# Optimization experiments

Measured on AMD Instinct MI355X. Metric: run time of the kernel, lower is better.

Reference implementation:

```python
import jax, jax.numpy as jnp
import numpy as np

N, E, F_IN, G = 50000, 800000, 128, 256
LAYERS = [(128, 4, 64), (256, 4, 64), (256, 1, 64)]  # (fan_in, heads, per-head dim)


def setup_inputs() -> dict:
    key = jax.random.key(0)
    ks = iter(jax.random.split(key, 64))
    nrm = lambda shp, s=1.0: jax.random.normal(next(ks), shp, jnp.float32) * s
    d = {}
    d["x"] = nrm((N, F_IN))
    d["edge_index"] = jax.random.randint(next(ks), (2, E), 0, N, dtype=jnp.int32)
    d["batch"] = jnp.sort(jax.random.randint(next(ks), (N,), 0, G, dtype=jnp.int32))
    for i, (fin, h, c) in enumerate(LAYERS):
        d[f"w{i}"] = nrm((fin, h * c), 1.0 / np.sqrt(fin))
        d[f"asrc{i}"] = nrm((h, c), 0.1)
        d[f"adst{i}"] = nrm((h, c), 0.1)
        d[f"b{i}"] = nrm((h * c,), 0.1)
        d[f"g{i}"] = 1.0 + nrm((h * c,), 0.1)
        d[f"be{i}"] = nrm((h * c,), 0.1)
        d[f"m{i}"] = nrm((h * c,), 0.1)
        d[f"v{i}"] = jnp.abs(nrm((h * c,), 0.1)) + 1.0
    d["fc1w"] = nrm((192, 64), 1.0 / np.sqrt(192)); d["fc1b"] = nrm((64,), 0.1)
    d["fc2w"] = nrm((64, 32), 1.0 / np.sqrt(64));   d["fc2b"] = nrm((32,), 0.1)
    d["fc3w"] = nrm((32, 1), 1.0 / np.sqrt(32));    d["fc3b"] = nrm((1,), 0.1)
    return d


def _gat_layer(x, w, a_s, a_d, b, src, dst, n, heads):
    c = w.shape[1] // heads
    h = (x @ w).reshape(n, heads, c)                      # [N,H,C]
    al_s = jnp.sum(h * a_s[None], axis=-1)                # [N,H]
    al_d = jnp.sum(h * a_d[None], axis=-1)                # [N,H]
    e = jax.nn.leaky_relu(al_s[src] + al_d[dst], 0.2)     # [E',H]
    emax = jax.ops.segment_max(e, dst, num_segments=n)
    emax = jnp.where(jnp.isfinite(emax), emax, 0.0)
    ee = jnp.exp(e - emax[dst])
    den = jax.ops.segment_sum(ee, dst, num_segments=n)
    alpha = ee / (den[dst] + 1e-16)                       # edge softmax per dst node
    out = jax.ops.segment_sum(h[src] * alpha[..., None], dst, num_segments=n)
    return out.reshape(n, heads * c) + b


def _bn(x, g, be, m, v):
    return (x - m) * jax.lax.rsqrt(v + 1e-5) * g + be


def reference(x, edge_index, batch,
              w0, asrc0, adst0, b0, g0, be0, m0, v0,
              w1, asrc1, adst1, b1, g1, be1, m1, v1,
              w2, asrc2, adst2, b2, g2, be2, m2, v2,
              fc1w, fc1b, fc2w, fc2b, fc3w, fc3b):
    n = x.shape[0]
    loop = jnp.arange(n, dtype=edge_index.dtype)          # add_self_loops (PyG default)
    src = jnp.concatenate([edge_index[0], loop])
    dst = jnp.concatenate([edge_index[1], loop])
    layers = [(w0, asrc0, adst0, b0, g0, be0, m0, v0, 4),
              (w1, asrc1, adst1, b1, g1, be1, m1, v1, 4),
              (w2, asrc2, adst2, b2, g2, be2, m2, v2, 1)]
    for (w, a_s, a_d, b, g, be, m, v, heads) in layers:
        x = _gat_layer(x, w, a_s, a_d, b, src, dst, n, heads)
        x = jax.nn.elu(_bn(x, g, be, m, v))
    # multi-pool readout over graphs
    xsum = jax.ops.segment_sum(x, batch, num_segments=G)
    cnt = jax.ops.segment_sum(jnp.ones((n, 1), x.dtype), batch, num_segments=G)
    xmean = xsum / jnp.maximum(cnt, 1.0)
    xmax = jax.ops.segment_max(x, batch, num_segments=G)
    xmax = jnp.where(jnp.isfinite(xmax), xmax, 0.0)
    h = jnp.concatenate([xmean, xmax, xsum], axis=1)      # [G, 192]
    h = jax.nn.relu(h @ fc1w + fc1b)
    h = jax.nn.relu(h @ fc2w + fc2b)
    return h @ fc3w + fc3b                                # [G, 1]
```

## Files before the change

### kernel.cpp

```cpp
#include <hip/hip_runtime.h>
#include <hip/hip_fp16.h>

typedef unsigned short ushort_t;
typedef unsigned int uint_t;
typedef __attribute__((ext_vector_type(8))) _Float16 half8;
typedef __attribute__((ext_vector_type(4))) float f32x4;

#define NN 50000
#define NE 800000
#define NGR 256

typedef __attribute__((address_space(3))) unsigned int as3_u32;
typedef const __attribute__((address_space(1))) unsigned int as1_u32c;
__device__ __forceinline__ void gld16(const ushort_t* g, void* lds_base) {
    __builtin_amdgcn_global_load_lds((as1_u32c*)g, (as3_u32*)lds_base, 16, 0, 0);
}

__global__ void k_scan1(const int* __restrict__ deg, int* __restrict__ rowp,
                        int* __restrict__ bsum, int M) {
    __shared__ int sm[256];
    int t = threadIdx.x, i = blockIdx.x * 256 + t;
    int v = (i < M) ? deg[i] + 1 : 0;
    sm[t] = v; __syncthreads();
    for (int off = 1; off < 256; off <<= 1) {
        int x = (t >= off) ? sm[t - off] : 0;
        __syncthreads();
        sm[t] += x;
        __syncthreads();
    }
    if (i < M) rowp[i] = sm[t] - v;
    if (t == 255) bsum[blockIdx.x] = sm[255];
}

__global__ void k_scan2(int* bsum, int NB) {
    __shared__ int sm[256];
    int t = threadIdx.x;
    int v = (t < NB) ? bsum[t] : 0;
    sm[t] = v; __syncthreads();
    for (int off = 1; off < 256; off <<= 1) {
        int x = (t >= off) ? sm[t - off] : 0;
        __syncthreads();
        sm[t] += x;
        __syncthreads();
    }
    if (t < NB) bsum[t] = sm[t] - v;
}

__global__ void k_scan3(int* rowp, const int* __restrict__ bsum, int* __restrict__ cur,
                        int* __restrict__ colv, int M, int total) {
    int i = blockIdx.x * 256 + threadIdx.x;
    if (i < M) {
        int rp = rowp[i] + bsum[blockIdx.x];
        rowp[i] = rp;
        colv[rp] = i;
        cur[i] = rp + 1;
    }
    if (i == 0) rowp[M] = total;
}

__global__ void k_prep(const float* __restrict__ x0, __half* __restrict__ xf,
                       const float* __restrict__ W0, const float* __restrict__ W1,
                       const float* __restrict__ W2, __half* __restrict__ th,
                       const int* __restrict__ edst, int* __restrict__ deg) {
    int i = blockIdx.x * 256 + threadIdx.x;
    if (i < 1600000) {
        float4 v = ((const float4*)x0)[i];
        __half2 a = __floats2half2_rn(v.x, v.y);
        __half2 b = __floats2half2_rn(v.z, v.w);
        *(__half2*)(xf + i * 4) = a;
        *(__half2*)(xf + i * 4 + 2) = b;
    } else if (i < 1600000 + 114688) {
        int w = i - 1600000;
        const float* W; int K, NC, idx, base;
        if (w < 32768)      { W = W0; K = 128; NC = 256; idx = w;         base = 0; }
        else if (w < 98304) { W = W1; K = 256; NC = 256; idx = w - 32768; base = 32768; }
        else                { W = W2; K = 256; NC = 64;  idx = w - 98304; base = 98304; }
        int k = idx / NC, n = idx % NC;
        th[base + n * K + k] = __float2half(W[idx]);
    } else if (i < 1600000 + 114688 + NE) {
        atomicAdd(&deg[edst[i - 1714688]], 1);
    }
}

template<int KD, int BN>
__device__ __forceinline__ void gemm_body(int bx, int by,
    const __half* __restrict__ Ax, const __half* __restrict__ Bth,
    __half* __restrict__ Hout, const float* __restrict__ a_s,
    const float* __restrict__ a_d, float* __restrict__ als,
    float* __restrict__ ald, int H, int M, int NC) {
    constexpr int BM = 128, BK = 32;
    __shared__ ushort_t sA[BM * BK];
    __shared__ ushort_t sB[BN * BK];
    const int tid = threadIdx.x;
    const int m0 = bx * BM;
    const int n0 = by * BN;
    const int wv = tid >> 6, ln = tid & 63;
    const int lrow = ln & 15, lq = ln >> 4;
    constexpr int RT = (BN == 128) ? 4 : 2;
    int wm, wn;
    if constexpr (BN == 128) { wm = (wv >> 1) * 64; wn = (wv & 1) * 64; }
    else                     { wm = wv * 32;        wn = 0; }
    const int roff = ln >> 2;
    const int coff = (ln & 3) * 8;

    f32x4 acc[RT][4] = {};

    for (int k0 = 0; k0 < KD; k0 += BK) {
        #pragma unroll
        for (int ch = 0; ch < 2; ++ch) {
            int rb = wv * 32 + ch * 16;
            size_t ga = (size_t)(m0 + rb + roff) * KD + k0 + coff;
            gld16((const ushort_t*)Ax + ga, &sA[rb * BK]);
        }
        if constexpr (BN == 128) {
            #pragma unroll
            for (int ch = 0; ch < 2; ++ch) {
                int rb = wv * 32 + ch * 16;
                size_t gb = (size_t)(n0 + rb + roff) * KD + k0 + coff;
                gld16((const ushort_t*)Bth + gb, &sB[rb * BK]);
            }
        } else {
            int rb = wv * 16;
            size_t gb = (size_t)(n0 + rb + roff) * KD + k0 + coff;
            gld16((const ushort_t*)Bth + gb, &sB[rb * BK]);
        }
        __syncthreads();
        half8 af[RT], bf[4];
        #pragma unroll
        for (int r = 0; r < RT; ++r)
            af[r] = *(const half8*)&sA[(wm + r * 16 + lrow) * BK + lq * 8];
        #pragma unroll
        for (int c = 0; c < 4; ++c)
            bf[c] = *(const half8*)&sB[(wn + c * 16 + lrow) * BK + lq * 8];
        #pragma unroll
        for (int r = 0; r < RT; ++r)
            #pragma unroll
            for (int c = 0; c < 4; ++c)
                acc[r][c] = __builtin_amdgcn_mfma_f32_16x16x32_f16(af[r], bf[c], acc[r][c], 0, 0, 0);
        __syncthreads();
    }
    #pragma unroll
    for (int r = 0; r < RT; ++r) {
        #pragma unroll
        for (int c = 0; c < 4; ++c) {
            int colg = n0 + wn + c * 16 + lrow;
            #pragma unroll
            for (int j = 0; j < 4; ++j) {
                int row = m0 + wm + r * 16 + lq * 4 + j;
                if (row < M) Hout[(size_t)row * NC + colg] = __float2half(acc[r][c][j]);
            }
        }
    }
    int hh = (n0 + wn) >> 6;
    float asv[4], adv[4];
    #pragma unroll
    for (int c = 0; c < 4; ++c) {
        int cg = (n0 + wn + c * 16 + lrow) & 63;
        asv[c] = a_s[hh * 64 + cg];
        adv[c] = a_d[hh * 64 + cg];
    }
    #pragma unroll
    for (int r = 0; r < RT; ++r) {
        #pragma unroll
        for (int j = 0; j < 4; ++j) {
            float ts = 0.f, td = 0.f;
            #pragma unroll
            for (int c = 0; c < 4; ++c) {
                float v = acc[r][c][j];
                ts += v * asv[c];
                td += v * adv[c];
            }
            #pragma unroll
            for (int m = 1; m < 16; m <<= 1) {
                ts += __shfl_xor(ts, m);
                td += __shfl_xor(td, m);
            }
            int row = m0 + wm + r * 16 + lq * 4 + j;
            if (lrow == 0 && row < M) {
                als[row * H + hh] = ts;
                ald[row * H + hh] = td;
            }
        }
    }
}

template<int KD, int BN>
__global__ __launch_bounds__(256)
void k_mgemm(const __half* __restrict__ Ax, const __half* __restrict__ Bth,
             __half* __restrict__ Hout,
             const float* __restrict__ a_s, const float* __restrict__ a_d,
             float* __restrict__ als, float* __restrict__ ald,
             int H, int M, int NC) {
    gemm_body<KD, BN>(blockIdx.x, blockIdx.y, Ax, Bth, Hout, a_s, a_d, als, ald, H, M, NC);
}

__global__ __launch_bounds__(256)
void k_gf(const __half* __restrict__ Ax, const __half* __restrict__ Bth,
          __half* __restrict__ Hout,
          const float* __restrict__ a_s, const float* __restrict__ a_d,
          float* __restrict__ als, float* __restrict__ ald, int M,
          const int* __restrict__ esrc, const int* __restrict__ edst,
          int* __restrict__ cur, int* __restrict__ colv) {
    if (blockIdx.x < 782) {
        gemm_body<128, 128>(blockIdx.x >> 1, blockIdx.x & 1, Ax, Bth, Hout,
                            a_s, a_d, als, ald, 4, M, 256);
    } else {
        int fid = blockIdx.x - 782;
        int r = blockIdx.x & 7;
        int c = fid >> 3;
        int base = c * 1024 + (int)threadIdx.x * 4;
        if (base < NE) {
            int4 dv = *(const int4*)(edst + base);
            int4 sv = *(const int4*)(esrc + base);
            const int lo = r * 6250;
            const int* dp = (const int*)&dv;
            const int* sp = (const int*)&sv;
            #pragma unroll
            for (int j = 0; j < 4; ++j) {
                int d = dp[j];
                if ((unsigned)(d - lo) < 6250u) {
                    int pos = atomicAdd(&cur[d], 1);
                    colv[pos] = sp[j];
                }
            }
        }
    }
}

template<int H>
__global__ __launch_bounds__(256)
void k_att(const float* __restrict__ als, const float* __restrict__ ald,
           const int* __restrict__ rowp, const int* __restrict__ colv,
           __half* __restrict__ alpha, float* __restrict__ invb, int M) {
    int node = blockIdx.x * 16 + (threadIdx.x >> 4);
    if (node >= M) return;
    int l = threadIdx.x & 15;
    int rs = rowp[node], re = rowp[node + 1];
    if constexpr (H == 4) {
        float4 ad = *(const float4*)(ald + node * 4);
        float d0 = 0.f, d1 = 0.f, d2 = 0.f, d3 = 0.f;
        for (int i = rs + l; i < re; i += 16) {
            int s = colv[i];
            float4 av = *(const float4*)(als + s * 4);
            float e0 = av.x + ad.x; e0 = e0 > 0.f ? e0 : 0.2f * e0; e0 = __expf(e0);
            float e1 = av.y + ad.y; e1 = e1 > 0.f ? e1 : 0.2f * e1; e1 = __expf(e1);
            float e2 = av.z + ad.z; e2 = e2 > 0.f ? e2 : 0.2f * e2; e2 = __expf(e2);
            float e3 = av.w + ad.w; e3 = e3 > 0.f ? e3 : 0.2f * e3; e3 = __expf(e3);
            d0 += e0; d1 += e1; d2 += e2; d3 += e3;
            __half2 p0 = __floats2half2_rn(e0, e1);
            __half2 p1 = __floats2half2_rn(e2, e3);
            uint2 pk;
            pk.x = *(uint_t*)&p0; pk.y = *(uint_t*)&p1;
            *(uint2*)(alpha + (size_t)i * 4) = pk;
        }
        #pragma unroll
        for (int off = 1; off < 16; off <<= 1) {
            d0 += __shfl_xor(d0, off); d1 += __shfl_xor(d1, off);
            d2 += __shfl_xor(d2, off); d3 += __shfl_xor(d3, off);
        }
        if (l == 0)
            *(float4*)(invb + node * 4) = make_float4(1.f / (d0 + 1e-16f), 1.f / (d1 + 1e-16f),
                                                      1.f / (d2 + 1e-16f), 1.f / (d3 + 1e-16f));
    } else {
        float ad = ald[node];
        float d = 0.f;
        for (int i = rs + l; i < re; i += 16) {
            int s = colv[i];
            float e = als[s] + ad; e = e > 0.f ? e : 0.2f * e; e = __expf(e);
            d += e;
            alpha[i] = __float2half(e);
        }
        #pragma unroll
        for (int off = 1; off < 16; off <<= 1) d += __shfl_xor(d, off);
        if (l == 0) invb[node] = 1.f / (d + 1e-16f);
    }
}

template<int H, bool SPLIT>
__global__ __launch_bounds__(256)
void k_agg(const __half* __restrict__ h, const __half* __restrict__ alpha,
           const float* __restrict__ invb, const int* __restrict__ rowp,
           const int* __restrict__ colv,
           const float* __restrict__ bias, const float* __restrict__ gam,
           const float* __restrict__ bet, const float* __restrict__ mu,
           const float* __restrict__ var,
           __half* __restrict__ xo, float* __restrict__ xf, int M) {
    constexpr int HC = H * 64;
    constexpr int EG = 512 / HC;
    constexpr int L  = 64 / EG;
    constexpr int UN = (H == 4) ? 4 : 2;
    int node = blockIdx.x * 4 + (threadIdx.x >> 6);
    if (node >= M) return;
    int lane = threadIdx.x & 63;
    int rs = rowp[node], re = rowp[node + 1];
    int l = lane & (L - 1), eg = lane / L;
    int hB = (l * 8) >> 6;
    const ushort_t* ab = (const ushort_t*)alpha;
    float acc[8] = {};
    for (int i = rs; i < re; i += EG * UN) {
        #pragma unroll
        for (int k = 0; k < UN; ++k) {
            int idx = i + eg + k * EG;
            bool vld = idx < re;
            int idx2 = vld ? idx : rs;
            int s = colv[idx2];
            ushort_t abits;
            if constexpr (H == 4) abits = ab[(size_t)idx2 * 4 + hB];
            else                  abits = ab[idx2];
            float a = __half2float(__ushort_as_half(vld ? abits : (ushort_t)0));
            uint4 hv = *(const uint4*)(h + (size_t)s * HC + l * 8);
            const __half* hp = (const __half*)&hv;
            #pragma unroll
            for (int j = 0; j < 8; ++j)
                acc[j] = fmaf(a, __half2float(hp[j]), acc[j]);
        }
    }
    #pragma unroll
    for (int off = L; off < 64; off <<= 1) {
        #pragma unroll
        for (int j = 0; j < 8; ++j) acc[j] += __shfl_xor(acc[j], off);
    }
    if (eg == 0) {
        float inv = (H == 4) ? invb[node * 4 + hB] : invb[node];
        float fo[8];
        #pragma unroll
        for (int j = 0; j < 8; ++j) {
            int d = l * 8 + j;
            float o = acc[j] * inv + bias[d];
            float bn = (o - mu[d]) * rsqrtf(var[d] + 1e-5f) * gam[d] + bet[d];
            fo[j] = bn > 0.f ? bn : (__expf(bn) - 1.f);
        }
        if constexpr (SPLIT) {
            __half2 p0 = __floats2half2_rn(fo[0], fo[1]);
            __half2 p1 = __floats2half2_rn(fo[2], fo[3]);
            __half2 p2 = __floats2half2_rn(fo[4], fo[5]);
            __half2 p3 = __floats2half2_rn(fo[6], fo[7]);
            uint4 pk;
            pk.x = *(uint_t*)&p0; pk.y = *(uint_t*)&p1;
            pk.z = *(uint_t*)&p2; pk.w = *(uint_t*)&p3;
            *(uint4*)&xo[(size_t)node * HC + l * 8] = pk;
        } else {
            *(float4*)&xf[(size_t)node * HC + l * 8] = make_float4(fo[0], fo[1], fo[2], fo[3]);
            *(float4*)&xf[(size_t)node * HC + l * 8 + 4] = make_float4(fo[4], fo[5], fo[6], fo[7]);
        }
    }
}

__global__ __launch_bounds__(512)
void k_poolfc(const float* __restrict__ x, const int* __restrict__ batch,
              const float* __restrict__ fc1w, const float* __restrict__ fc1b,
              const float* __restrict__ fc2w, const float* __restrict__ fc2b,
              const float* __restrict__ fc3w, const float* __restrict__ fc3b,
              float* __restrict__ out, int M) {
    __shared__ float ssum[8][64];
    __shared__ float smax[8][64];
    __shared__ float hb[192];
    __shared__ float h1[64];
    __shared__ float h2[32];
    int g = blockIdx.x, t = threadIdx.x;
    int d = t & 63, sub = t >> 6;
    int lo = 0, hi = M;
    while (lo < hi) { int mid = (lo + hi) >> 1; if (batch[mid] < g) lo = mid + 1; else hi = mid; }
    int s = lo;
    lo = 0; hi = M;
    while (lo < hi) { int mid = (lo + hi) >> 1; if (batch[mid] < g + 1) lo = mid + 1; else hi = mid; }
    int e = lo;
    float sum = 0.f, mx = -3.0e38f;
    for (int n = s + sub; n < e; n += 8) {
        float v = x[(size_t)n * 64 + d];
        sum += v; mx = fmaxf(mx, v);
    }
    ssum[sub][d] = sum; smax[sub][d] = mx;
    __syncthreads();
    if (t < 64) {
        float sm = 0.f, m2 = -3.0e38f;
        #pragma unroll
        for (int k = 0; k < 8; ++k) { sm += ssum[k][t]; m2 = fmaxf(m2, smax[k][t]); }
        int cnt = e - s;
        hb[t] = sm / (float)(cnt > 1 ? cnt : 1);
        hb[64 + t] = (cnt == 0) ? 0.f : m2;
        hb[128 + t] = sm;
    }
    __syncthreads();
    if (t < 64) {
        float s1 = fc1b[t];
        for (int k = 0; k < 192; ++k) s1 += hb[k] * fc1w[k * 64 + t];
        h1[t] = fmaxf(s1, 0.f);
    }
    __syncthreads();
    if (t < 32) {
        float s2 = fc2b[t];
        for (int k = 0; k < 64; ++k) s2 += h1[k] * fc2w[k * 32 + t];
        h2[t] = fmaxf(s2, 0.f);
    }
    __syncthreads();
    if (t == 0) {
        float s3 = fc3b[0];
        for (int k = 0; k < 32; ++k) s3 += h2[k] * fc3w[k];
        out[g] = s3;
    }
}

extern "C" void kernel_launch(void* const* d_in, const int* in_sizes, int n_in,
                              void* d_out, int out_size, void* d_ws, size_t ws_size,
                              hipStream_t stream) {
    const float* x0     = (const float*)d_in[0];
    const int* ei       = (const int*)d_in[1];
    const int* batch    = (const int*)d_in[2];
    const float* W[3]   = {(const float*)d_in[3],  (const float*)d_in[11], (const float*)d_in[19]};
    const float* AS[3]  = {(const float*)d_in[4],  (const float*)d_in[12], (const float*)d_in[20]};
    const float* AD[3]  = {(const float*)d_in[5],  (const float*)d_in[13], (const float*)d_in[21]};
    const float* BI[3]  = {(const float*)d_in[6],  (const float*)d_in[14], (const float*)d_in[22]};
    const float* GA[3]  = {(const float*)d_in[7],  (const float*)d_in[15], (const float*)d_in[23]};
    const float* BE[3]  = {(const float*)d_in[8],  (const float*)d_in[16], (const float*)d_in[24]};
    const float* MU[3]  = {(const float*)d_in[9],  (const float*)d_in[17], (const float*)d_in[25]};
    const float* VA[3]  = {(const float*)d_in[10], (const float*)d_in[18], (const float*)d_in[26]};
    const float* fc1w = (const float*)d_in[27];
    const float* fc1b = (const float*)d_in[28];
    const float* fc2w = (const float*)d_in[29];
    const float* fc2b = (const float*)d_in[30];
    const float* fc3w = (const float*)d_in[31];
    const float* fc3b = (const float*)d_in[32];

    char* ws = (char*)d_ws;
    int*   rowp   = (int*)  (ws);
    int*   colv   = (int*)  (ws + 200704);
    int*   bsum   = (int*)  (ws + 3600704);
    float* als    = (float*)(ws + 3602432);
    float* ald    = (float*)(ws + 4402432);
    __half* wTh   = (__half*)(ws + 5202432);
    __half* h_buf = (__half*)(ws + 5661184);
    __half* xf16  = (__half*)(ws + 31261184);
    float* xpool  = (float*)(ws + 56885760);
    __half* alpha = (__half*)(ws + 69685760);
    float* invb   = (float*)(ws + 83285760);
    int*   cur    = (int*)  (ws + 84085760);

    const int* esrc = ei;
    const int* edst = ei + NE;
    const int NB_SCAN = (NN + 255) / 256;

    hipMemsetAsync(cur, 0, NN * sizeof(int), stream);
    k_prep<<<(1600000 + 114688 + NE + 255) / 256, 256, 0, stream>>>(x0, xf16, W[0], W[1], W[2],
                                                                    wTh, edst, cur);
    k_scan1<<<NB_SCAN, 256, 0, stream>>>(cur, rowp, bsum, NN);
    k_scan2<<<1, 256, 0, stream>>>(bsum, NB_SCAN);
    k_scan3<<<NB_SCAN, 256, 0, stream>>>(rowp, bsum, cur, colv, NN, NE + NN);

    const int GB = (NN + 127) / 128;
    const int FILLB = ((NE + 1023) / 1024) * 8;
    int nwb = (NN + 3) / 4;
    int nab = (NN + 15) / 16;

    k_gf<<<782 + FILLB, 256, 0, stream>>>(xf16, wTh, h_buf, AS[0], AD[0], als, ald, NN,
                                          esrc, edst, cur, colv);
    k_att<4><<<nab, 256, 0, stream>>>(als, ald, rowp, colv, alpha, invb, NN);
    k_agg<4, true><<<nwb, 256, 0, stream>>>(h_buf, alpha, invb, rowp, colv,
                                            BI[0], GA[0], BE[0], MU[0], VA[0],
                                            xf16, nullptr, NN);
    k_mgemm<256, 128><<<dim3(GB, 2), 256, 0, stream>>>(xf16, wTh + 32768, h_buf,
                                                       AS[1], AD[1], als, ald, 4, NN, 256);
    k_att<4><<<nab, 256, 0, stream>>>(als, ald, rowp, colv, alpha, invb, NN);
    k_agg<4, true><<<nwb, 256, 0, stream>>>(h_buf, alpha, invb, rowp, colv,
                                            BI[1], GA[1], BE[1], MU[1], VA[1],
                                            xf16, nullptr, NN);
    k_mgemm<256, 64><<<dim3(GB, 1), 256, 0, stream>>>(xf16, wTh + 98304, h_buf,
                                                      AS[2], AD[2], als, ald, 1, NN, 64);
    k_att<1><<<nab, 256, 0, stream>>>(als, ald, rowp, colv, alpha, invb, NN);
    k_agg<1, false><<<nwb, 256, 0, stream>>>(h_buf, alpha, invb, rowp, colv,
                                             BI[2], GA[2], BE[2], MU[2], VA[2],
                                             nullptr, xpool, NN);

    k_poolfc<<<NGR, 512, 0, stream>>>(xpool, batch, fc1w, fc1b, fc2w, fc2b, fc3w, fc3b,
                                      (float*)d_out, NN);
    (void)in_sizes; (void)n_in; (void)out_size; (void)ws_size;
}
```

Measured before the change: 459.4 us.

## Restructure GAT aggregation to full-wavefront rows with readlane-broadcast edge indices

The aggregation kernel now assigns the whole 64-lane wavefront to one node's feature row instead of splitting lanes into edge groups. Each batch of up to 64 neighbour indices and attention weights is loaded cooperatively, then broadcast lane by lane with readlane, with 8 gathers in flight at a time. This removes the cross-lane shuffle reduction and the redundant per-lane colv/alpha loads, but makes each lane's gather narrower (8 or 2 bytes) and puts edges in series within a wavefront. The SPLIT template path is dropped: H==4 always writes half output and H==1 always writes float output.

```diff
diff --git a/kernel.cpp b/kernel.cpp
--- a/kernel.cpp
+++ b/kernel.cpp
@@ -286,63 +286,112 @@
            const float* __restrict__ var,
            __half* __restrict__ xo, float* __restrict__ xf, int M) {
     constexpr int HC = H * 64;
-    constexpr int EG = 512 / HC;
-    constexpr int L  = 64 / EG;
-    constexpr int UN = (H == 4) ? 4 : 2;
     int node = blockIdx.x * 4 + (threadIdx.x >> 6);
     if (node >= M) return;
-    int lane = threadIdx.x & 63;
+    int l = threadIdx.x & 63;
     int rs = rowp[node], re = rowp[node + 1];
-    int l = lane & (L - 1), eg = lane / L;
-    int hB = (l * 8) >> 6;
-    const ushort_t* ab = (const ushort_t*)alpha;
-    float acc[8] = {};
-    for (int i = rs; i < re; i += EG * UN) {
-        #pragma unroll
-        for (int k = 0; k < UN; ++k) {
-            int idx = i + eg + k * EG;
-            bool vld = idx < re;
-            int idx2 = vld ? idx : rs;
-            int s = colv[idx2];
-            ushort_t abits;
-            if constexpr (H == 4) abits = ab[(size_t)idx2 * 4 + hB];
-            else                  abits = ab[idx2];
-            float a = __half2float(__ushort_as_half(vld ? abits : (ushort_t)0));
-            uint4 hv = *(const uint4*)(h + (size_t)s * HC + l * 8);
-            const __half* hp = (const __half*)&hv;
-            #pragma unroll
-            for (int j = 0; j < 8; ++j)
-                acc[j] = fmaf(a, __half2float(hp[j]), acc[j]);
-        }
-    }
-    #pragma unroll
-    for (int off = L; off < 64; off <<= 1) {
-        #pragma unroll
-        for (int j = 0; j < 8; ++j) acc[j] += __shfl_xor(acc[j], off);
-    }
-    if (eg == 0) {
-        float inv = (H == 4) ? invb[node * 4 + hB] : invb[node];
-        float fo[8];
-        #pragma unroll
-        for (int j = 0; j < 8; ++j) {
-            int d = l * 8 + j;
-            float o = acc[j] * inv + bias[d];
-            float bn = (o - mu[d]) * rsqrtf(var[d] + 1e-5f) * gam[d] + bet[d];
+    float acc[H] = {};
+
+    for (int base = rs; base < re; base += 64) {
+        int nrem = re - base; if (nrem > 64) nrem = 64;
+        int pidx = base + l; if (pidx >= re) pidx = re - 1;
+        int cv = colv[pidx];
+        uint_t aw0 = 0, aw1 = 0;
+        if constexpr (H == 4) {
+            uint2 av = *(const uint2*)(alpha + (size_t)pidx * 4);
+            aw0 = av.x; aw1 = av.y;
+        } else {
+            aw0 = ((const ushort_t*)alpha)[pidx];
+        }
+        int e = 0;
+        for (; e + 8 <= nrem; e += 8) {
+            int sv[8]; uint_t w0[8], w1[8];
+            #pragma unroll
+            for (int u = 0; u < 8; ++u) {
+                sv[u] = __builtin_amdgcn_readlane(cv, e + u);
+                w0[u] = (uint_t)__builtin_amdgcn_readlane((int)aw0, e + u);
+                if constexpr (H == 4)
+                    w1[u] = (uint_t)__builtin_amdgcn_readlane((int)aw1, e + u);
+            }
+            if constexpr (H == 4) {
+                uint2 hv[8];
+                #pragma unroll
+                for (int u = 0; u < 8; ++u)
+                    hv[u] = *(const uint2*)(h + (size_t)sv[u] * 256 + l * 4);
+                #pragma unroll
+                for (int u = 0; u < 8; ++u) {
+                    uint_t aw = (l < 32) ? w0[u] : w1[u];
+                    aw = (l & 16) ? (aw >> 16) : (aw & 0xffffu);
+                    float af = __half2float(__ushort_as_half((ushort_t)aw));
+                    const __half* hp = (const __half*)&hv[u];
+                    #pragma unroll
+                    for (int j = 0; j < 4; ++j)
+                        acc[j] = fmaf(af, __half2float(hp[j]), acc[j]);
+                }
+            } else {
+                ushort_t hv[8];
+                #pragma unroll
+                for (int u = 0; u < 8; ++u)
+                    hv[u] = ((const ushort_t*)h)[(size_t)sv[u] * 64 + l];
+                #pragma unroll
+                for (int u = 0; u < 8; ++u) {
+                    float af = __half2float(__ushort_as_half((ushort_t)(w0[u] & 0xffffu)));
+                    acc[0] = fmaf(af, __half2float(__ushort_as_half(hv[u])), acc[0]);
+                }
+            }
+        }
+        for (; e < nrem; ++e) {
+            int s = __builtin_amdgcn_readlane(cv, e);
+            uint_t w0s = (uint_t)__builtin_amdgcn_readlane((int)aw0, e);
+            if constexpr (H == 4) {
+                uint_t w1s = (uint_t)__builtin_amdgcn_readlane((int)aw1, e);
+                uint_t aw = (l < 32) ? w0s : w1s;
+                aw = (l & 16) ? (aw >> 16) : (aw & 0xffffu);
+                float af = __half2float(__ushort_as_half((ushort_t)aw));
+                uint2 hv = *(const uint2*)(h + (size_t)s * 256 + l * 4);
+                const __half* hp = (const __half*)&hv;
+                #pragma unroll
+                for (int j = 0; j < 4; ++j)
+                    acc[j] = fmaf(af, __half2float(hp[j]), acc[j]);
+            } else {
+                float af = __half2float(__ushort_as_half((ushort_t)(w0s & 0xffffu)));
+                float hf = __half2float(((const __half*)h)[(size_t)s * 64 + l]);
+                acc[0] = fmaf(af, hf, acc[0]);
+            }
+        }
+    }
+
+    if constexpr (H == 4) {
+        int head = l >> 4;
+        float inv = invb[node * 4 + head];
+        float4 bi = *(const float4*)(bias + l * 4);
+        float4 ga = *(const float4*)(gam + l * 4);
+        float4 be = *(const float4*)(bet + l * 4);
+        float4 m4 = *(const float4*)(mu + l * 4);
+        float4 v4 = *(const float4*)(var + l * 4);
+        float bp[4] = {bi.x, bi.y, bi.z, bi.w};
+        float gp[4] = {ga.x, ga.y, ga.z, ga.w};
+        float ep[4] = {be.x, be.y, be.z, be.w};
+        float mp[4] = {m4.x, m4.y, m4.z, m4.w};
+        float vp[4] = {v4.x, v4.y, v4.z, v4.w};
+        float fo[4];
+        #pragma unroll
+        for (int j = 0; j < 4; ++j) {
+            float o = acc[j] * inv + bp[j];
+            float bn = (o - mp[j]) * rsqrtf(vp[j] + 1e-5f) * gp[j] + ep[j];
             fo[j] = bn > 0.f ? bn : (__expf(bn) - 1.f);
         }
-        if constexpr (SPLIT) {
-            __half2 p0 = __floats2half2_rn(fo[0], fo[1]);
-            __half2 p1 = __floats2half2_rn(fo[2], fo[3]);
-            __half2 p2 = __floats2half2_rn(fo[4], fo[5]);
-            __half2 p3 = __floats2half2_rn(fo[6], fo[7]);
-            uint4 pk;
-            pk.x = *(uint_t*)&p0; pk.y = *(uint_t*)&p1;
-            pk.z = *(uint_t*)&p2; pk.w = *(uint_t*)&p3;
-            *(uint4*)&xo[(size_t)node * HC + l * 8] = pk;
-        } else {
-            *(float4*)&xf[(size_t)node * HC + l * 8] = make_float4(fo[0], fo[1], fo[2], fo[3]);
-            *(float4*)&xf[(size_t)node * HC + l * 8 + 4] = make_float4(fo[4], fo[5], fo[6], fo[7]);
-        }
+        __half2 p0 = __floats2half2_rn(fo[0], fo[1]);
+        __half2 p1 = __floats2half2_rn(fo[2], fo[3]);
+        uint2 pk;
+        pk.x = *(uint_t*)&p0; pk.y = *(uint_t*)&p1;
+        *(uint2*)&xo[(size_t)node * 256 + l * 4] = pk;
+    } else {
+        float inv = invb[node];
+        float o = acc[0] * inv + bias[l];
+        float bn = (o - mu[l]) * rsqrtf(var[l] + 1e-5f) * gam[l] + bet[l];
+        float fo = bn > 0.f ? bn : (__expf(bn) - 1.f);
+        xf[(size_t)node * 64 + l] = fo;
     }
 }
 
```

After: 456.9 us. About the same (-0.6%).
